# Optimization experiments

Measured on AMD Instinct MI355X. Metric: run time of the kernel, lower is better.

## Reference

```python
import jax, jax.numpy as jnp
import numpy as np
from jax import lax

# Static problem sizes (see shape_source)
B, C, N = 32, 512, 64
SENTS_PER_VIDEO = 4
TARGETS_PER_SENT = 2
S = B * SENTS_PER_VIDEO          # 128 sentences
M = S * TARGETS_PER_SENT         # 256 target moments
P = N * (N + 1) // 2             # 2080 valid proposals (upper-tri mask2d)
T_TEMP = 0.1
MARGIN = 0.0
NEG_IOU = 0.5
K_TOP = 1                        # pos_topk
WEIGHT = 1.0


def setup_inputs() -> dict:
    key = jax.random.key(0)
    k1, k2, k3, k4 = jax.random.split(key, 4)
    return {
        "video_feats": jax.random.normal(k1, (B, C, N, N), jnp.float32),
        "sents_feats": jax.random.normal(k2, (S, C), jnp.float32),
        "num_sentences": jnp.full((B,), SENTS_PER_VIDEO, jnp.int32),
        "num_targets": jnp.full((S,), TARGETS_PER_SENT, jnp.int32),
        "iou2d": jax.random.uniform(k3, (S, N, N), jnp.float32),
        "iou2ds": jax.random.uniform(k4, (M, N, N), jnp.float32),
        "mask2d": jnp.triu(jnp.ones((N, N), bool)),
        "epoch": 0,  # < start_DNS_epoch -> DNS branch skipped
    }


def _log_cross_entropy(pos_scores, all_scores, neg_mask, t, m):
    # Faithful to LogCrossEntropy.forward
    pos_exp = jnp.exp((pos_scores - m) / t)
    neg_exp_sum = jnp.sum(jnp.exp(all_scores / t) * neg_mask, axis=-1)
    loss = -((pos_scores - m) / t - jnp.log(pos_exp + neg_exp_sum))
    return jnp.mean(loss)


def _l2_normalize(x, axis=-1, eps=1e-12):
    n = jnp.linalg.norm(x, axis=axis, keepdims=True)
    return x / jnp.maximum(n, eps)


def reference(video_feats, sents_feats, num_sentences, num_targets,
              iou2d, iou2ds, mask2d, epoch):
    # Compact valid proposals (P is static: upper-triangular mask2d)
    idx = jnp.nonzero(mask2d.reshape(-1), size=P)[0]              # (P,)
    v = video_feats.reshape(B, C, N * N)[:, :, idx]               # (B,C,P)
    v = jnp.transpose(v, (0, 2, 1))                               # (B,P,C)
    iou2d_f = iou2d.reshape(S, N * N)[:, idx]                     # (S,P)
    iou2ds_f = iou2ds.reshape(M, N * N)[:, idx]                   # (M,P)

    v = _l2_normalize(v)
    sents = _l2_normalize(sents_feats)

    scatter_s2v = jnp.repeat(jnp.arange(B), num_sentences, total_repeat_length=S)
    scatter_m2s = jnp.repeat(jnp.arange(S), num_targets, total_repeat_length=M)
    scatter_m2v = scatter_s2v[scatter_m2s]

    # top-K proposals per target moment by IoU
    topk_idx = lax.top_k(iou2ds_f, K_TOP)[1]                      # (M,K)
    topk_v = jnp.take_along_axis(v[scatter_m2v], topk_idx[:, :, None], axis=1)  # (M,K,C)

    # inter-video loss
    inter_video_pos = jnp.einsum('mkc,mc->mk', topk_v, sents[scatter_m2s])  # (M,K)
    inter_video_all = jnp.einsum('mkc,sc->mks', topk_v, sents)              # (M,K,S)
    inter_video_neg_mask = (~jnp.eye(S, dtype=bool))[scatter_m2s][:, None, :]  # (M,1,S)
    loss_inter_video = _log_cross_entropy(
        inter_video_pos, inter_video_all, inter_video_neg_mask, T_TEMP, MARGIN)

    # inter-query loss
    inter_query_pos = inter_video_pos                              # (M,K)
    inter_query_all = (sents @ v.reshape(B * P, C).T)[:, None, :]  # (S,1,B*P)
    # pos_mask: block-diagonal per video, refined by IoU > neg_iou inside own block
    onehot = jnp.eye(B, dtype=bool)[scatter_s2v]                   # (S,B)
    pos_mask = (onehot[:, :, None] & (iou2d_f > NEG_IOU)[:, None, :]).reshape(S, B * P)
    inter_query_neg_mask = (~pos_mask)[:, None, :]                 # (S,1,B*P)
    loss_inter_query = _log_cross_entropy(
        inter_query_pos, inter_query_all[scatter_m2s],
        inter_query_neg_mask[scatter_m2s], T_TEMP, MARGIN)

    total = (loss_inter_video + loss_inter_query) * WEIGHT
    return total, loss_inter_video, loss_inter_query
```

## Files before the change

kernel.cpp:

```cpp
#include <hip/hip_runtime.h>
#include <cstdint>

#define BB 32
#define CC 512
#define NSQ 4096
#define SS 128
#define MM 256
#define PP 2080
#define JJ (BB*PP)
#define NBIG (JJ/128)

#define WS_SN     0
#define WS_SNB    262144
#define WS_IDX    393216
#define WS_IV     401536
#define WS_PART   532608

typedef short bf16x8 __attribute__((ext_vector_type(8)));
typedef float f32x4  __attribute__((ext_vector_type(4)));

__device__ __forceinline__ unsigned short f2bf(float x) {
    unsigned int u = __float_as_uint(x);
    unsigned int r = (u + 0x7fffu + ((u >> 16) & 1u)) >> 16;
    return (unsigned short)r;
}

__global__ void k_prep(const float* __restrict__ sents, float* __restrict__ sn,
                       unsigned short* __restrict__ snb, int* __restrict__ idx) {
    const int blk = blockIdx.x, t = threadIdx.x;
    if (blk < 128) {
        __shared__ float red[256];
        const float* row = sents + (size_t)blk * CC;
        float x0 = row[t], x1 = row[t + 256];
        red[t] = x0 * x0 + x1 * x1;
        __syncthreads();
        for (int off = 128; off > 0; off >>= 1) {
            if (t < off) red[t] += red[t + off];
            __syncthreads();
        }
        float rn = 1.0f / fmaxf(sqrtf(red[0]), 1e-12f);
        float y0 = x0 * rn, y1 = x1 * rn;
        sn[(size_t)blk * CC + t]        = y0;
        sn[(size_t)blk * CC + t + 256]  = y1;
        snb[(size_t)blk * CC + t]       = f2bf(y0);
        snb[(size_t)blk * CC + t + 256] = f2bf(y1);
    } else {
        int i = (blk - 128) * 256 + t;
        int r = i >> 6, c = i & 63;
        if (c >= r) {
            int p = r * 64 - (r * (r - 1)) / 2 + (c - r);
            idx[p] = i;
        }
    }
}


union SMem {
    struct {
        unsigned short sA[128 * 64];
        unsigned short vB[128 * 64];
        int   colb[128];
        int   colflat[128];
        float colrn[128];
        float sqpart[256];
    } big;
    struct {
        float sv[256];
        int   si[256];
        float tvs[512];
        float red[256];
    } fus;
};

__global__ __launch_bounds__(256, 2)
void k_mega(const float* __restrict__ video, const float* __restrict__ sn,
            const unsigned short* __restrict__ snb,
            const float* __restrict__ iou2d, const float* __restrict__ iou2ds,
            const int* __restrict__ idx,
            float* __restrict__ iv, float* __restrict__ part) {
    __shared__ SMem sm;
    const int t = threadIdx.x;

    if (blockIdx.x < MM) {
        const int m = blockIdx.x;
        {
            float best = -1e30f; int bi = 1 << 30;
            const float* row = iou2ds + (size_t)m * NSQ;
            for (int p = t; p < PP; p += 256) {
                float v = row[idx[p]];
                if (v > best || (v == best && p < bi)) { best = v; bi = p; }
            }
            sm.fus.sv[t] = best; sm.fus.si[t] = bi;
            __syncthreads();
            for (int off = 128; off > 0; off >>= 1) {
                if (t < off) {
                    float v2 = sm.fus.sv[t + off]; int i2 = sm.fus.si[t + off];
                    if (v2 > sm.fus.sv[t] || (v2 == sm.fus.sv[t] && i2 < sm.fus.si[t])) {
                        sm.fus.sv[t] = v2; sm.fus.si[t] = i2;
                    }
                }
                __syncthreads();
            }
        }
        const int flat = idx[sm.fus.si[0]];
        const int b = m >> 3;

        const float* base = video + (size_t)b * CC * NSQ + flat;
        float x0 = base[(size_t)t * NSQ];
        float x1 = base[(size_t)(t + 256) * NSQ];
        sm.fus.red[t] = x0 * x0 + x1 * x1;
        __syncthreads();
        for (int off = 128; off > 0; off >>= 1) {
            if (t < off) sm.fus.red[t] += sm.fus.red[t + off];
            __syncthreads();
        }
        float rn = 1.0f / fmaxf(sqrtf(sm.fus.red[0]), 1e-12f);
        sm.fus.tvs[t] = x0 * rn;
        sm.fus.tvs[t + 256] = x1 * rn;
        __syncthreads();

        const int s = t & 127, h = t >> 7;
        const float4* a4 = (const float4*)(sm.fus.tvs + h * 256);
        const float4* b4 = (const float4*)(sn + (size_t)s * CC + h * 256);
        float acc = 0.f;
#pragma unroll 8
        for (int c = 0; c < 64; c++) {
            float4 a = a4[c], bb = b4[c];
            acc += a.x * bb.x + a.y * bb.y + a.z * bb.z + a.w * bb.w;
        }
        __syncthreads();
        sm.fus.red[t] = acc;
        __syncthreads();
        if (t < 128) iv[(size_t)m * SS + t] = sm.fus.red[t] + sm.fus.red[t + 128];
        return;
    }

    const int w    = t >> 6;
    const int lane = t & 63;
    const int q    = lane >> 4;
    const int l15  = lane & 15;
    const int bid  = blockIdx.x - MM;
    const int j0   = bid * 128;

    if (t < 128) {
        int col = j0 + t;
        int b = col / PP;
        sm.big.colb[t] = b;
        sm.big.colflat[t] = idx[col - b * PP];
    }

    const int G_    = t & 7;
    const int rowA0 = t >> 3;
    const int swzA  = ((G_ ^ (rowA0 & 7)) * 8);
    const int jj = t & 127;
    const int kh = t >> 7;
    int colL = j0 + jj;
    int bL = colL / PP;
    int flatL = idx[colL - bL * PP];
    const float* vbase = video + (size_t)bL * (CC * NSQ) + flatL
                               + (size_t)(kh * 32) * NSQ;
    const unsigned short* snbA = snb + (size_t)rowA0 * CC + G_ * 8;
    unsigned short* sAp = sm.big.sA + rowA0 * 64 + swzA;
    unsigned short* vBp = sm.big.vB + jj * 64;
    const int jj7 = jj & 7;

    bf16x8 prA[4];
    float  pr[32];
#pragma unroll
    for (int it = 0; it < 4; it++)
        prA[it] = *(const bf16x8*)(snbA + (size_t)it * 32 * CC);
#pragma unroll
    for (int i = 0; i < 32; i++) pr[i] = vbase[(size_t)i * NSQ];

    f32x4 acc[2][8];
#pragma unroll
    for (int i = 0; i < 2; i++)
#pragma unroll
        for (int j = 0; j < 8; j++) acc[i][j] = (f32x4){0.f, 0.f, 0.f, 0.f};

    float sqa = 0.f;

    for (int k0 = 0; k0 < CC; k0 += 64) {
#pragma unroll
        for (int it = 0; it < 4; it++)
            *(bf16x8*)(sAp + it * 32 * 64) = prA[it];
#pragma unroll
        for (int g = 0; g < 4; g++) {
            unsigned short buf[8];
#pragma unroll
            for (int i = 0; i < 8; i++) {
                float x = pr[g * 8 + i];
                sqa += x * x;
                buf[i] = f2bf(x);
            }
            int Gb = kh * 4 + g;
            *(bf16x8*)(vBp + ((Gb ^ jj7) * 8)) = *(bf16x8*)buf;
        }
        __syncthreads();

        if (k0 + 64 < CC) {
            const int kn = k0 + 64;
#pragma unroll
            for (int it = 0; it < 4; it++)
                prA[it] = *(const bf16x8*)(snbA + (size_t)it * 32 * CC + kn);
            const float* vp = vbase + (size_t)kn * NSQ;
#pragma unroll
            for (int i = 0; i < 32; i++) pr[i] = vp[(size_t)i * NSQ];
        }

#pragma unroll
        for (int ks = 0; ks < 64; ks += 32) {
            const int so = (((ks >> 3) + q) ^ (l15 & 7)) * 8;
            bf16x8 a[2], bfr[8];
#pragma unroll
            for (int rt = 0; rt < 2; rt++) {
                int row = w * 32 + rt * 16 + l15;
                a[rt] = *(const bf16x8*)(sm.big.sA + row * 64 + so);
            }
#pragma unroll
            for (int ct = 0; ct < 8; ct++) {
                int col = ct * 16 + l15;
                bfr[ct] = *(const bf16x8*)(sm.big.vB + col * 64 + so);
            }
#pragma unroll
            for (int rt = 0; rt < 2; rt++)
#pragma unroll
                for (int ct = 0; ct < 8; ct++)
                    acc[rt][ct] = __builtin_amdgcn_mfma_f32_16x16x32_bf16(
                        a[rt], bfr[ct], acc[rt][ct], 0, 0, 0);
        }
        __syncthreads();
    }

    sm.big.sqpart[t] = sqa;
    __syncthreads();
    if (t < 128)
        sm.big.colrn[t] = 1.0f / fmaxf(sqrtf(sm.big.sqpart[t] + sm.big.sqpart[t + 128]), 1e-12f);
    __syncthreads();

    float crn[8]; int cb[8], cf[8];
#pragma unroll
    for (int ct = 0; ct < 8; ct++) {
        int c = ct * 16 + l15;
        crn[ct] = sm.big.colrn[c];
        cb[ct]  = sm.big.colb[c];
        cf[ct]  = sm.big.colflat[c];
    }
#pragma unroll
    for (int rt = 0; rt < 2; rt++) {
#pragma unroll
        for (int r = 0; r < 4; r++) {
            int s = w * 32 + rt * 16 + q * 4 + r;
            float rowsum = 0.f;
#pragma unroll
            for (int ct = 0; ct < 8; ct++) {
                float sc = acc[rt][ct][r] * crn[ct];
                float e = __expf(sc * 10.0f);
                if ((s >> 2) == cb[ct]) {
                    if (iou2d[(size_t)s * NSQ + cf[ct]] > 0.5f) e = 0.f;
                }
                rowsum += e;
            }
#pragma unroll
            for (int msk = 1; msk < 16; msk <<= 1)
                rowsum += __shfl_xor(rowsum, msk, 64);
            if (l15 == 0) part[(size_t)bid * 128 + s] = rowsum;
        }
    }
}

__global__ void k_final(const float* __restrict__ iv, const float* __restrict__ part,
                        float* __restrict__ out) {
    const int t = threadIdx.x;
    __shared__ float nqs[256];
    __shared__ float rv[256], rq[256];
    {
        const int sl = t & 127, h = t >> 7;
        float nq = 0.f;
        for (int j = h; j < NBIG; j += 2) nq += part[(size_t)j * 128 + sl];
        nqs[t] = nq;
    }
    __syncthreads();
    const float* row = iv + (size_t)t * SS;
    const int ms = t >> 1;
    float pos = row[ms];
    float nv = 0.f;
    for (int s = 0; s < SS; s++) {
        float e = expf(row[s] * 10.0f);
        if (s == ms) e = 0.f;
        nv += e;
    }
    float pe = expf(pos * 10.0f);
    float negq_ms = nqs[ms] + nqs[ms + 128];
    float lv = logf(pe + nv) - pos * 10.0f;
    float lq = logf(pe + negq_ms) - pos * 10.0f;
    rv[t] = lv; rq[t] = lq;
    __syncthreads();
    for (int off = 128; off > 0; off >>= 1) {
        if (t < off) { rv[t] += rv[t + off]; rq[t] += rq[t + off]; }
        __syncthreads();
    }
    if (t == 0) {
        float liv = rv[0] / 256.f, liq = rq[0] / 256.f;
        out[0] = liv + liq;
        out[1] = liv;
        out[2] = liq;
    }
}

extern "C" void kernel_launch(void* const* d_in, const int* in_sizes, int n_in,
                              void* d_out, int out_size, void* d_ws, size_t ws_size,
                              hipStream_t stream) {
    const float* video  = (const float*)d_in[0];
    const float* sents  = (const float*)d_in[1];
    const float* iou2d  = (const float*)d_in[4];
    const float* iou2ds = (const float*)d_in[5];
    float* out = (float*)d_out;

    char* ws = (char*)d_ws;
    float*          sn   = (float*)(ws + WS_SN);
    unsigned short* snb  = (unsigned short*)(ws + WS_SNB);
    int*            idx  = (int*)(ws + WS_IDX);
    float*          iv   = (float*)(ws + WS_IV);
    float*          part = (float*)(ws + WS_PART);

    k_prep <<<144, 256, 0, stream>>>(sents, sn, snb, idx);
    k_mega <<<MM + NBIG, 256, 0, stream>>>(video, sn, snb, iou2d, iou2ds, idx, iv, part);
    k_final<<<1, 256, 0, stream>>>(iv, part, out);
}
```

Before: 481.2 us.

## Tile GEMM over dense 64x64 positions with coalesced float4 video loads and masking

Drops the compacted proposal index and tiles the video-sentence GEMM over all N*N positions per video, 128 contiguous positions per block. Video features are now loaded as coalesced float4 rows rather than gathered scalars, and lower-triangle positions are zeroed in the epilogue. The cost is roughly twice as much GEMM work and video traffic, since invalid positions are computed too. The LDS swizzle also changes to an XOR over two 3-bit fields, and the part buffer layout changes with the new block count.

```diff
diff --git a/kernel.cpp b/kernel.cpp
--- a/kernel.cpp
+++ b/kernel.cpp
@@ -1,4 +1,5 @@
 #include <hip/hip_runtime.h>
+#include <hip/hip_bf16.h>
 #include <cstdint>
 
 #define BB 32
@@ -6,15 +7,13 @@
 #define NSQ 4096
 #define SS 128
 #define MM 256
-#define PP 2080
-#define JJ (BB*PP)
-#define NBIG (JJ/128)
-
-#define WS_SN     0
-#define WS_SNB    262144
-#define WS_IDX    393216
-#define WS_IV     401536
-#define WS_PART   532608
+#define NTILE 32
+#define NBIG (BB*NTILE)
+
+#define WS_SN   0
+#define WS_SNB  262144
+#define WS_IV   393216
+#define WS_PART 524288
 
 typedef short bf16x8 __attribute__((ext_vector_type(8)));
 typedef float f32x4  __attribute__((ext_vector_type(4)));
@@ -25,33 +24,30 @@
     return (unsigned short)r;
 }
 
+__device__ __forceinline__ unsigned pk2(float a, float b) {
+    union { __hip_bfloat162 h; unsigned u; } cv;
+    cv.h = __float22bfloat162_rn(make_float2(a, b));
+    return cv.u;
+}
+
 __global__ void k_prep(const float* __restrict__ sents, float* __restrict__ sn,
-                       unsigned short* __restrict__ snb, int* __restrict__ idx) {
+                       unsigned short* __restrict__ snb) {
     const int blk = blockIdx.x, t = threadIdx.x;
-    if (blk < 128) {
-        __shared__ float red[256];
-        const float* row = sents + (size_t)blk * CC;
-        float x0 = row[t], x1 = row[t + 256];
-        red[t] = x0 * x0 + x1 * x1;
-        __syncthreads();
-        for (int off = 128; off > 0; off >>= 1) {
-            if (t < off) red[t] += red[t + off];
-            __syncthreads();
-        }
-        float rn = 1.0f / fmaxf(sqrtf(red[0]), 1e-12f);
-        float y0 = x0 * rn, y1 = x1 * rn;
-        sn[(size_t)blk * CC + t]        = y0;
-        sn[(size_t)blk * CC + t + 256]  = y1;
-        snb[(size_t)blk * CC + t]       = f2bf(y0);
-        snb[(size_t)blk * CC + t + 256] = f2bf(y1);
-    } else {
-        int i = (blk - 128) * 256 + t;
-        int r = i >> 6, c = i & 63;
-        if (c >= r) {
-            int p = r * 64 - (r * (r - 1)) / 2 + (c - r);
-            idx[p] = i;
-        }
-    }
+    __shared__ float red[256];
+    const float* row = sents + (size_t)blk * CC;
+    float x0 = row[t], x1 = row[t + 256];
+    red[t] = x0 * x0 + x1 * x1;
+    __syncthreads();
+    for (int off = 128; off > 0; off >>= 1) {
+        if (t < off) red[t] += red[t + off];
+        __syncthreads();
+    }
+    float rn = 1.0f / fmaxf(sqrtf(red[0]), 1e-12f);
+    float y0 = x0 * rn, y1 = x1 * rn;
+    sn[(size_t)blk * CC + t]        = y0;
+    sn[(size_t)blk * CC + t + 256]  = y1;
+    snb[(size_t)blk * CC + t]       = f2bf(y0);
+    snb[(size_t)blk * CC + t + 256] = f2bf(y1);
 }
 
 
@@ -59,10 +55,8 @@
     struct {
         unsigned short sA[128 * 64];
         unsigned short vB[128 * 64];
-        int   colb[128];
-        int   colflat[128];
+        float sqred[8][128];
         float colrn[128];
-        float sqpart[256];
     } big;
     struct {
         float sv[256];
@@ -76,7 +70,6 @@
 void k_mega(const float* __restrict__ video, const float* __restrict__ sn,
             const unsigned short* __restrict__ snb,
             const float* __restrict__ iou2d, const float* __restrict__ iou2ds,
-            const int* __restrict__ idx,
             float* __restrict__ iv, float* __restrict__ part) {
     __shared__ SMem sm;
     const int t = threadIdx.x;
@@ -86,9 +79,10 @@
         {
             float best = -1e30f; int bi = 1 << 30;
             const float* row = iou2ds + (size_t)m * NSQ;
-            for (int p = t; p < PP; p += 256) {
-                float v = row[idx[p]];
-                if (v > best || (v == best && p < bi)) { best = v; bi = p; }
+            for (int pos = t; pos < NSQ; pos += 256) {
+                float v = row[pos];
+                bool valid = (pos & 63) >= (pos >> 6);
+                if (valid && (v > best || (v == best && pos < bi))) { best = v; bi = pos; }
             }
             sm.fus.sv[t] = best; sm.fus.si[t] = bi;
             __syncthreads();
@@ -102,7 +96,7 @@
                 __syncthreads();
             }
         }
-        const int flat = idx[sm.fus.si[0]];
+        const int flat = sm.fus.si[0];
         const int b = m >> 3;
 
         const float* base = video + (size_t)b * CC * NSQ + flat;
@@ -140,37 +134,21 @@
     const int q    = lane >> 4;
     const int l15  = lane & 15;
     const int bid  = blockIdx.x - MM;
-    const int j0   = bid * 128;
-
-    if (t < 128) {
-        int col = j0 + t;
-        int b = col / PP;
-        sm.big.colb[t] = b;
-        sm.big.colflat[t] = idx[col - b * PP];
-    }
-
-    const int G_    = t & 7;
-    const int rowA0 = t >> 3;
-    const int swzA  = ((G_ ^ (rowA0 & 7)) * 8);
-    const int jj = t & 127;
-    const int kh = t >> 7;
-    int colL = j0 + jj;
-    int bL = colL / PP;
-    int flatL = idx[colL - bL * PP];
-    const float* vbase = video + (size_t)bL * (CC * NSQ) + flatL
-                               + (size_t)(kh * 32) * NSQ;
-    const unsigned short* snbA = snb + (size_t)rowA0 * CC + G_ * 8;
-    unsigned short* sAp = sm.big.sA + rowA0 * 64 + swzA;
-    unsigned short* vBp = sm.big.vB + jj * 64;
-    const int jj7 = jj & 7;
-
+    const int b    = bid >> 5;
+    const int pos0 = (bid & 31) * 128;
+
+    const int tg = t & 31;
+    const int cg = t >> 5;
+    const float* vbase = video + ((size_t)b * CC + cg * 8) * NSQ + pos0 + tg * 4;
+    const unsigned short* snbA = snb + (size_t)(t >> 3) * CC + (t & 7) * 8;
+
+    float4 prB[8];
     bf16x8 prA[4];
-    float  pr[32];
+#pragma unroll
+    for (int i = 0; i < 8; i++) prB[i] = *(const float4*)(vbase + (size_t)i * NSQ);
 #pragma unroll
     for (int it = 0; it < 4; it++)
         prA[it] = *(const bf16x8*)(snbA + (size_t)it * 32 * CC);
-#pragma unroll
-    for (int i = 0; i < 32; i++) pr[i] = vbase[(size_t)i * NSQ];
 
     f32x4 acc[2][8];
 #pragma unroll
@@ -178,49 +156,58 @@
 #pragma unroll
         for (int j = 0; j < 8; j++) acc[i][j] = (f32x4){0.f, 0.f, 0.f, 0.f};
 
-    float sqa = 0.f;
+    float sq4[4] = {0.f, 0.f, 0.f, 0.f};
 
     for (int k0 = 0; k0 < CC; k0 += 64) {
 #pragma unroll
-        for (int it = 0; it < 4; it++)
-            *(bf16x8*)(sAp + it * 32 * 64) = prA[it];
-#pragma unroll
-        for (int g = 0; g < 4; g++) {
-            unsigned short buf[8];
-#pragma unroll
-            for (int i = 0; i < 8; i++) {
-                float x = pr[g * 8 + i];
-                sqa += x * x;
-                buf[i] = f2bf(x);
-            }
-            int Gb = kh * 4 + g;
-            *(bf16x8*)(vBp + ((Gb ^ jj7) * 8)) = *(bf16x8*)buf;
+        for (int it = 0; it < 4; it++) {
+            int row = (t >> 3) + it * 32;
+            int sw = (((t & 7) ^ (row & 7) ^ ((row >> 3) & 7)) & 7) * 8;
+            *(bf16x8*)(sm.big.sA + row * 64 + sw) = prA[it];
+        }
+#pragma unroll
+        for (int p = 0; p < 4; p++) {
+            int pos = tg * 4 + p;
+            union { float4 v; float f[4]; } u0, u1, u2, u3, u4, u5, u6, u7;
+            u0.v = prB[0]; u1.v = prB[1]; u2.v = prB[2]; u3.v = prB[3];
+            u4.v = prB[4]; u5.v = prB[5]; u6.v = prB[6]; u7.v = prB[7];
+            float v0 = u0.f[p], v1 = u1.f[p], v2 = u2.f[p], v3 = u3.f[p];
+            float v4 = u4.f[p], v5 = u5.f[p], v6 = u6.f[p], v7 = u7.f[p];
+            sq4[p] += v0 * v0 + v1 * v1 + v2 * v2 + v3 * v3
+                    + v4 * v4 + v5 * v5 + v6 * v6 + v7 * v7;
+            unsigned uu[4];
+            uu[0] = pk2(v0, v1); uu[1] = pk2(v2, v3);
+            uu[2] = pk2(v4, v5); uu[3] = pk2(v6, v7);
+            int sw = ((cg ^ (pos & 7) ^ ((pos >> 3) & 7)) & 7) * 8;
+            *(bf16x8*)(sm.big.vB + pos * 64 + sw) = *(bf16x8*)uu;
         }
         __syncthreads();
 
         if (k0 + 64 < CC) {
             const int kn = k0 + 64;
 #pragma unroll
+            for (int i = 0; i < 8; i++)
+                prB[i] = *(const float4*)(vbase + (size_t)(kn + i) * NSQ);
+#pragma unroll
             for (int it = 0; it < 4; it++)
                 prA[it] = *(const bf16x8*)(snbA + (size_t)it * 32 * CC + kn);
-            const float* vp = vbase + (size_t)kn * NSQ;
-#pragma unroll
-            for (int i = 0; i < 32; i++) pr[i] = vp[(size_t)i * NSQ];
         }
 
 #pragma unroll
         for (int ks = 0; ks < 64; ks += 32) {
-            const int so = (((ks >> 3) + q) ^ (l15 & 7)) * 8;
+            const int G = (ks >> 3) + q;
             bf16x8 a[2], bfr[8];
 #pragma unroll
             for (int rt = 0; rt < 2; rt++) {
                 int row = w * 32 + rt * 16 + l15;
-                a[rt] = *(const bf16x8*)(sm.big.sA + row * 64 + so);
+                int sw = ((G ^ (row & 7) ^ ((row >> 3) & 7)) & 7) * 8;
+                a[rt] = *(const bf16x8*)(sm.big.sA + row * 64 + sw);
             }
 #pragma unroll
             for (int ct = 0; ct < 8; ct++) {
                 int col = ct * 16 + l15;
-                bfr[ct] = *(const bf16x8*)(sm.big.vB + col * 64 + so);
+                int sw = ((G ^ (col & 7) ^ ((col >> 3) & 7)) & 7) * 8;
+                bfr[ct] = *(const bf16x8*)(sm.big.vB + col * 64 + sw);
             }
 #pragma unroll
             for (int rt = 0; rt < 2; rt++)
@@ -232,33 +219,33 @@
         __syncthreads();
     }
 
-    sm.big.sqpart[t] = sqa;
-    __syncthreads();
-    if (t < 128)
-        sm.big.colrn[t] = 1.0f / fmaxf(sqrtf(sm.big.sqpart[t] + sm.big.sqpart[t + 128]), 1e-12f);
-    __syncthreads();
-
-    float crn[8]; int cb[8], cf[8];
-#pragma unroll
-    for (int ct = 0; ct < 8; ct++) {
-        int c = ct * 16 + l15;
-        crn[ct] = sm.big.colrn[c];
-        cb[ct]  = sm.big.colb[c];
-        cf[ct]  = sm.big.colflat[c];
-    }
+#pragma unroll
+    for (int p = 0; p < 4; p++) sm.big.sqred[cg][tg * 4 + p] = sq4[p];
+    __syncthreads();
+    if (t < 128) {
+        float s2 = 0.f;
+#pragma unroll
+        for (int g = 0; g < 8; g++) s2 += sm.big.sqred[g][t];
+        sm.big.colrn[t] = 1.0f / fmaxf(sqrtf(s2), 1e-12f);
+    }
+    __syncthreads();
+
+    float crn[8];
+#pragma unroll
+    for (int ct = 0; ct < 8; ct++) crn[ct] = sm.big.colrn[ct * 16 + l15];
 #pragma unroll
     for (int rt = 0; rt < 2; rt++) {
 #pragma unroll
         for (int r = 0; r < 4; r++) {
             int s = w * 32 + rt * 16 + q * 4 + r;
+            bool match = ((s >> 2) == b);
             float rowsum = 0.f;
 #pragma unroll
             for (int ct = 0; ct < 8; ct++) {
-                float sc = acc[rt][ct][r] * crn[ct];
-                float e = __expf(sc * 10.0f);
-                if ((s >> 2) == cb[ct]) {
-                    if (iou2d[(size_t)s * NSQ + cf[ct]] > 0.5f) e = 0.f;
-                }
+                int pos = pos0 + ct * 16 + l15;
+                float e = __expf(acc[rt][ct][r] * crn[ct] * 10.0f);
+                if (match && iou2d[(size_t)s * NSQ + pos] > 0.5f) e = 0.f;
+                if ((pos & 63) < (pos >> 6)) e = 0.f;
                 rowsum += e;
             }
 #pragma unroll
@@ -320,11 +307,10 @@
     char* ws = (char*)d_ws;
     float*          sn   = (float*)(ws + WS_SN);
     unsigned short* snb  = (unsigned short*)(ws + WS_SNB);
-    int*            idx  = (int*)(ws + WS_IDX);
     float*          iv   = (float*)(ws + WS_IV);
     float*          part = (float*)(ws + WS_PART);
 
-    k_prep <<<144, 256, 0, stream>>>(sents, sn, snb, idx);
-    k_mega <<<MM + NBIG, 256, 0, stream>>>(video, sn, snb, iou2d, iou2ds, idx, iv, part);
+    k_prep <<<128, 256, 0, stream>>>(sents, sn, snb);
+    k_mega <<<MM + NBIG, 256, 0, stream>>>(video, sn, snb, iou2d, iou2ds, iv, part);
     k_final<<<1, 256, 0, stream>>>(iv, part, out);
 }
```

Result: slower. 521.2 us (+8.3%).
